# Kernel optimization log

Hardware: AMD Instinct MI355X
Metric: run time of the kernel (lower is better)

The kernel has to match this reference:

```python
import jax, jax.numpy as jnp
import numpy as np

N, E = 50000, 1600000
D_IN, D_HID, D_OUT = 256, 256, 128  # 2*output_dim = 256, output_dim = 128


def glorot(key, shape):
    fan_in, fan_out = shape
    limit = np.sqrt(6.0 / (fan_in + fan_out)).astype(np.float32)
    return jax.random.uniform(key, shape, jnp.float32, -limit, limit)


def setup_inputs() -> dict:
    key = jax.random.key(0)
    k0, k1, k2, k3 = jax.random.split(key, 4)
    x = jax.random.normal(k0, (N, D_IN), jnp.float32)
    edge_index = jax.random.randint(k1, (2, E), 0, N, jnp.int32)
    W1 = glorot(k2, (D_IN, D_HID))
    b1 = jnp.zeros((D_HID,), jnp.float32)
    W2 = glorot(k3, (D_HID, D_OUT))
    b2 = jnp.zeros((D_OUT,), jnp.float32)
    return {"x": x, "edge_index": edge_index, "W1": W1, "b1": b1, "W2": W2, "b2": b2}


def gcn_propagate(x, src, dst, num_nodes):
    """One hop of D^-1/2 (A + I) D^-1/2 @ x (PyG gcn_norm with self-loops)."""
    loops = jnp.arange(num_nodes, dtype=src.dtype)
    src_sl = jnp.concatenate([src, loops])  # [E + N]
    dst_sl = jnp.concatenate([dst, loops])
    ones = jnp.ones(src_sl.shape, x.dtype)
    deg = jax.ops.segment_sum(ones, dst_sl, num_segments=num_nodes)  # >= 1 (self-loop)
    dinv = jax.lax.rsqrt(jnp.maximum(deg, 1e-12))
    norm = dinv[src_sl] * dinv[dst_sl]  # [E + N]
    msgs = x[src_sl] * norm[:, None]    # gather + scale, [E+N, D]
    return jax.ops.segment_sum(msgs, dst_sl, num_segments=num_nodes)


def reference(x, edge_index, W1, b1, W2, b2):
    src, dst = edge_index[0], edge_index[1]
    n = x.shape[0]
    # SGConv(K=1): propagate then linear. conv1 + ReLU
    h = jax.nn.relu(gcn_propagate(x, src, dst, n) @ W1 + b1)
    # conv2 (GAE branch)
    return gcn_propagate(h, src, dst, n) @ W2 + b2
```

## Files before the change

### kernel.cpp

```cpp
#include <hip/hip_runtime.h>

typedef short s16x8 __attribute__((ext_vector_type(8)));
typedef float f32x4 __attribute__((ext_vector_type(4)));
typedef float f32x2 __attribute__((ext_vector_type(2)));

#define TILE 2048

__device__ __forceinline__ unsigned int brne(float f) {
    unsigned int u = __float_as_uint(f);
    return (u + 0x7FFFu + ((u >> 16) & 1u)) >> 16;
}
__device__ __forceinline__ float blo(unsigned int u) { return __uint_as_float(u << 16); }
__device__ __forceinline__ float bhi(unsigned int u) { return __uint_as_float(u & 0xFFFF0000u); }

__device__ __forceinline__ unsigned int pk_bf16(float lo, float hi) {
    unsigned int r;
    asm("v_cvt_pk_bf16_f32 %0, %1, %2" : "=v"(r) : "v"(lo), "v"(hi));
    return r;
}

__device__ __forceinline__ void pkfma(f32x2& a, const f32x2 x, const f32x2 w) {
    asm("v_pk_fma_f32 %0, %1, %2, %0" : "+v"(a) : "v"(x), "v"(w));
}

__device__ __forceinline__ void acc8p(f32x2* a, const uint4 u, const f32x2 w2) {
    pkfma(a[0], (f32x2){blo(u.x), bhi(u.x)}, w2);
    pkfma(a[1], (f32x2){blo(u.y), bhi(u.y)}, w2);
    pkfma(a[2], (f32x2){blo(u.z), bhi(u.z)}, w2);
    pkfma(a[3], (f32x2){blo(u.w), bhi(u.w)}, w2);
}

__device__ __forceinline__ void acc16p(f32x2* a, const uint4 u, const f32x2 w2) {
    pkfma(a[0], __builtin_amdgcn_cvt_pk_f32_fp8((int)u.x, false), w2);
    pkfma(a[1], __builtin_amdgcn_cvt_pk_f32_fp8((int)u.x, true),  w2);
    pkfma(a[2], __builtin_amdgcn_cvt_pk_f32_fp8((int)u.y, false), w2);
    pkfma(a[3], __builtin_amdgcn_cvt_pk_f32_fp8((int)u.y, true),  w2);
    pkfma(a[4], __builtin_amdgcn_cvt_pk_f32_fp8((int)u.z, false), w2);
    pkfma(a[5], __builtin_amdgcn_cvt_pk_f32_fp8((int)u.z, true),  w2);
    pkfma(a[6], __builtin_amdgcn_cvt_pk_f32_fp8((int)u.w, false), w2);
    pkfma(a[7], __builtin_amdgcn_cvt_pk_f32_fp8((int)u.w, true),  w2);
}


__global__ void k_bhist(const int* __restrict__ dst, int* __restrict__ bucket_cnt,
                        int e, int nb) {
    __shared__ int h[256];
    const int tid = threadIdx.x;
    h[tid] = 0;
    __syncthreads();
    const int base = blockIdx.x * TILE + tid;
#pragma unroll
    for (int k = 0; k < 8; k++) {
        const int i = base + k * 256;
        if (i < e) atomicAdd(&h[dst[i] >> 8], 1);
    }
    __syncthreads();
    if (tid < nb && h[tid]) atomicAdd(&bucket_cnt[tid], h[tid]);
}

__global__ void k_bscatter(const int* __restrict__ src, const int* __restrict__ dst,
                           const int* __restrict__ bcnt, int* __restrict__ bbase,
                           int* __restrict__ bcur, uint2* __restrict__ eb, int e, int nb) {
    __shared__ int sh[256], sbase[256], h[256], hbase[256], h2[256];
    const int tid = threadIdx.x;
    const int v = (tid < nb) ? bcnt[tid] : 0;
    int x = v;
    sh[tid] = x;
    __syncthreads();
    for (int off = 1; off < 256; off <<= 1) {
        const int t = (tid >= off) ? sh[tid - off] : 0;
        __syncthreads();
        if (tid >= off) { x += t; sh[tid] = x; }
        __syncthreads();
    }
    sbase[tid] = x - v;
    if (blockIdx.x == 0) {
        if (tid < nb) bbase[tid] = x - v;
        if (tid == 0) bbase[nb] = e;
    }
    h[tid] = 0; h2[tid] = 0;
    __syncthreads();
    const int base = blockIdx.x * TILE + tid;
    int s[8], d[8], b[8];
    bool val[8];
#pragma unroll
    for (int k = 0; k < 8; k++) {
        const int i = base + k * 256;
        val[k] = i < e;
        if (val[k]) {
            s[k] = src[i]; d[k] = dst[i]; b[k] = d[k] >> 8;
            atomicAdd(&h[b[k]], 1);
        }
    }
    __syncthreads();
    if (h[tid]) hbase[tid] = sbase[tid] + atomicAdd(&bcur[tid], h[tid]);
    __syncthreads();
#pragma unroll
    for (int k = 0; k < 8; k++) {
        if (val[k]) {
            const int off = atomicAdd(&h2[b[k]], 1);
            eb[hbase[b[k]] + off] = make_uint2((unsigned)s[k], (unsigned)d[k]);
        }
    }
}

__global__ void k_nhist_scan(const uint2* __restrict__ eb, const int* __restrict__ bucket_base,
                             int* __restrict__ rowptr, int* __restrict__ part,
                             float* __restrict__ dinv, int n) {
    __shared__ int c[256], sh[256];
    const int tid = threadIdx.x, b = blockIdx.x;
    c[tid] = 0;
    __syncthreads();
    const int beg = bucket_base[b], end = bucket_base[b + 1];
    for (int i = beg + tid; i < end; i += 256)
        atomicAdd(&c[eb[i].y & 255], 1);
    __syncthreads();
    const int v = c[tid];
    const int node = b * 256 + tid;
    if (node < n) dinv[node] = rsqrtf((float)(v + 1));
    int x = v;
    sh[tid] = x;
    __syncthreads();
    for (int off = 1; off < 256; off <<= 1) {
        const int t = (tid >= off) ? sh[tid - off] : 0;
        __syncthreads();
        if (tid >= off) { x += t; sh[tid] = x; }
        __syncthreads();
    }
    if (node <= n) rowptr[node] = x - v;
    if (tid == 255) part[b] = x;
}

template <bool PREW>
__global__ void k_place(const uint2* __restrict__ eb, const int* __restrict__ bucket_base,
                        int* __restrict__ rowptr, const int* __restrict__ part,
                        void* __restrict__ esv, const float* __restrict__ dinv,
                        int n, int nb, int e) {
    __shared__ int sh[256], rp[256], offs[256];
    __shared__ float sdv[256];
    const int tid = threadIdx.x, b = blockIdx.x;
    int x = (tid < nb) ? part[tid] : 0;
    sh[tid] = x;
    __syncthreads();
    for (int off = 1; off < 256; off <<= 1) {
        const int t = (tid >= off) ? sh[tid - off] : 0;
        __syncthreads();
        if (tid >= off) { x += t; sh[tid] = x; }
        __syncthreads();
    }
    const int prefix = (b > 0) ? sh[b - 1] : 0;
    const int node = b * 256 + tid;
    int rg = 0;
    if (node <= n) {
        rg = rowptr[node] + prefix;
        rowptr[node] = rg;
    }
    rp[tid] = rg;
    offs[tid] = 0;
    if (PREW) sdv[tid] = (node < n) ? dinv[node] : 0.f;
    __syncthreads();
    const int beg = bucket_base[b], end = bucket_base[b + 1];
    if (PREW) {
        int2* es2 = (int2*)esv;
        if (b == 0 && tid < 64) es2[e + tid] = make_int2(0, 0);
        for (int i = beg + tid; i < end; i += 256) {
            const uint2 ed = eb[i];
            const int sI = (int)ed.x, d = (int)ed.y & 255;
            const float w = dinv[sI] * sdv[d];
            const int local = atomicAdd(&offs[d], 1);
            es2[rp[d] + local] = make_int2(sI, __float_as_int(w));
        }
    } else {
        int* es1 = (int*)esv;
        for (int i = beg + tid; i < end; i += 256) {
            const uint2 ed = eb[i];
            const int d = (int)ed.y & 255;
            const int local = atomicAdd(&offs[d], 1);
            es1[rp[d] + local] = (int)ed.x;
        }
    }
}

__global__ void k_tW2(const float* __restrict__ W1, const float* __restrict__ W2,
                      unsigned short* __restrict__ W1t, unsigned short* __restrict__ W2t) {
    const int t = blockIdx.x * 256 + threadIdx.x;
    if (t < 65536) {
        const int k = t >> 8, nn = t & 255;
        W1t[nn * 256 + k] = (unsigned short)brne(W1[t]);
    } else {
        const int u = t - 65536;
        const int k = u >> 7, nn = u & 127;
        W2t[nn * 256 + k] = (unsigned short)brne(W2[u]);
    }
}

#define LP 40
template <bool AF32, bool FP8OUT>
__global__ __launch_bounds__(256) void k_gemm(const void* __restrict__ Av,
                                              const unsigned short* __restrict__ Bt,
                                              void* __restrict__ Cout,
                                              int M, int Nc) {
    __shared__ unsigned short As[2][128 * LP];
    __shared__ unsigned short Bs[2][128 * LP];

    const int tid = threadIdx.x;
    const int wave = tid >> 6, lane = tid & 63;
    const int wm = (wave >> 1) * 64, wn = (wave & 1) * 64;
    const int l15 = lane & 15, quad = lane >> 4;
    const int mBase = blockIdx.x * 128, nBase = blockIdx.y * 128;

    f32x4 acc[4][4];
#pragma unroll
    for (int i = 0; i < 4; i++)
#pragma unroll
        for (int j = 0; j < 4; j++) acc[i][j] = (f32x4){0.f, 0.f, 0.f, 0.f};

    const int r0 = tid >> 2, kc0 = tid & 3;
    int am0 = mBase + r0;      if (am0 >= M) am0 = M - 1;
    int am1 = mBase + r0 + 64; if (am1 >= M) am1 = M - 1;

    const uint4* Ap0; const uint4* Ap1; const float4* Af0; const float4* Af1;
    if (AF32) {
        Af0 = (const float4*)Av + (size_t)am0 * 64 + kc0 * 2;
        Af1 = (const float4*)Av + (size_t)am1 * 64 + kc0 * 2;
    } else {
        Ap0 = (const uint4*)Av + (size_t)am0 * 32 + kc0;
        Ap1 = (const uint4*)Av + (size_t)am1 * 32 + kc0;
    }
    const uint4* Bp0 = (const uint4*)Bt + (size_t)(nBase + r0) * 32 + kc0;
    const uint4* Bp1 = (const uint4*)Bt + (size_t)(nBase + r0 + 64) * 32 + kc0;

    uint4 a0, a1, b0, b1;
    auto LOAD = [&](int kt) {
        if (AF32) {
            const float4 l0 = Af0[kt * 8], h0 = Af0[kt * 8 + 1];
            const float4 l1 = Af1[kt * 8], h1 = Af1[kt * 8 + 1];
            a0.x = pk_bf16(l0.x, l0.y); a0.y = pk_bf16(l0.z, l0.w);
            a0.z = pk_bf16(h0.x, h0.y); a0.w = pk_bf16(h0.z, h0.w);
            a1.x = pk_bf16(l1.x, l1.y); a1.y = pk_bf16(l1.z, l1.w);
            a1.z = pk_bf16(h1.x, h1.y); a1.w = pk_bf16(h1.z, h1.w);
        } else {
            a0 = Ap0[kt * 4];
            a1 = Ap1[kt * 4];
        }
        b0 = Bp0[kt * 4];
        b1 = Bp1[kt * 4];
    };
    auto STORE = [&](int buf) {
        *(uint4*)&As[buf][r0 * LP + kc0 * 8] = a0;
        *(uint4*)&As[buf][(r0 + 64) * LP + kc0 * 8] = a1;
        *(uint4*)&Bs[buf][r0 * LP + kc0 * 8] = b0;
        *(uint4*)&Bs[buf][(r0 + 64) * LP + kc0 * 8] = b1;
    };

    LOAD(0);
    STORE(0);
    __syncthreads();
    for (int kt = 0; kt < 8; ++kt) {
        const int cur = kt & 1;
        if (kt < 7) LOAD(kt + 1);
        s16x8 af[4], bf[4];
#pragma unroll
        for (int i = 0; i < 4; i++)
            af[i] = *(const s16x8*)&As[cur][(wm + i * 16 + l15) * LP + quad * 8];
#pragma unroll
        for (int j = 0; j < 4; j++)
            bf[j] = *(const s16x8*)&Bs[cur][(wn + j * 16 + l15) * LP + quad * 8];
        if (kt < 7) STORE(cur ^ 1);
#pragma unroll
        for (int i = 0; i < 4; i++)
#pragma unroll
            for (int j = 0; j < 4; j++)
                acc[i][j] = __builtin_amdgcn_mfma_f32_16x16x32_bf16(af[i], bf[j], acc[i][j], 0, 0, 0);
        __syncthreads();
    }

#pragma unroll
    for (int i = 0; i < 4; i++) {
        const int rowb = mBase + wm + i * 16 + quad * 4;
#pragma unroll
        for (int j = 0; j < 4; j++) {
            const int col = nBase + wn + j * 16 + l15;
#pragma unroll
            for (int r = 0; r < 4; r += 2) {
                if (FP8OUT) {
                    const unsigned int pk = __builtin_amdgcn_cvt_pk_fp8_f32(
                        acc[i][j][r], acc[i][j][r + 1], 0, false);
                    if (rowb + r < M)
                        ((unsigned char*)Cout)[(size_t)(rowb + r) * Nc + col] =
                            (unsigned char)pk;
                    if (rowb + r + 1 < M)
                        ((unsigned char*)Cout)[(size_t)(rowb + r + 1) * Nc + col] =
                            (unsigned char)(pk >> 8);
                } else {
                    const unsigned int pk = pk_bf16(acc[i][j][r], acc[i][j][r + 1]);
                    if (rowb + r < M)
                        ((unsigned short*)Cout)[(size_t)(rowb + r) * Nc + col] =
                            (unsigned short)pk;
                    if (rowb + r + 1 < M)
                        ((unsigned short*)Cout)[(size_t)(rowb + r + 1) * Nc + col] =
                            (unsigned short)(pk >> 16);
                }
            }
        }
    }
}


template <bool PREW>
__global__ void k_prop256f8(const uint4* __restrict__ X4,
                            const int* __restrict__ rowptr,
                            const void* __restrict__ esv,
                            const float* __restrict__ dinv,
                            const float* __restrict__ bias,
                            uint4* __restrict__ Y4, int n) {
    const int wid = (int)((blockIdx.x * blockDim.x + threadIdx.x) >> 6);
    const int lane = threadIdx.x & 63;
    const int quad = lane >> 4, l16 = lane & 15;
    if (wid >= n) return;
    const float dd = dinv[wid];
    const int2* es2 = (const int2*)esv;
    const int*  es1 = (const int*)esv;
    f32x2 a[8];
#pragma unroll
    for (int k = 0; k < 8; k++) a[k] = (f32x2){0.f, 0.f};

    const int beg = rowptr[wid], end = rowptr[wid + 1];
    int j = beg + quad;

    auto EDGE = [&](int jj, int& s, float& w) {
        const bool v = jj < end;
        if (PREW) {
            const int2 p = es2[jj];
            s = p.x;
            w = v ? __int_as_float(p.y) : 0.f;
        } else {
            const int idx = v ? jj : 0;
            s = es1[idx];
            w = v ? dinv[s] * dd : 0.f;
        }
    };

    int s0, s1, s2, s3;
    float w0, w1, w2, w3;
    EDGE(j, s0, w0); EDGE(j + 4, s1, w1); EDGE(j + 8, s2, w2); EDGE(j + 12, s3, w3);

    if (quad == 0) {
        const uint4 v = X4[(size_t)wid * 16 + l16];
        acc16p(a, v, (f32x2){dd * dd, dd * dd});
    }

    while (j + 12 < end) {
        const uint4 u0 = X4[(size_t)s0 * 16 + l16];
        const uint4 u1 = X4[(size_t)s1 * 16 + l16];
        const uint4 u2 = X4[(size_t)s2 * 16 + l16];
        const uint4 u3 = X4[(size_t)s3 * 16 + l16];
        j += 16;
        int t0, t1, t2, t3;
        float x0, x1, x2, x3;
        EDGE(j, t0, x0); EDGE(j + 4, t1, x1); EDGE(j + 8, t2, x2); EDGE(j + 12, t3, x3);
        acc16p(a, u0, (f32x2){w0, w0});
        acc16p(a, u1, (f32x2){w1, w1});
        acc16p(a, u2, (f32x2){w2, w2});
        acc16p(a, u3, (f32x2){w3, w3});
        s0 = t0; s1 = t1; s2 = t2; s3 = t3;
        w0 = x0; w1 = x1; w2 = x2; w3 = x3;
    }
    {
        const uint4 u0 = X4[(size_t)s0 * 16 + l16];
        const uint4 u1 = X4[(size_t)s1 * 16 + l16];
        const uint4 u2 = X4[(size_t)s2 * 16 + l16];
        acc16p(a, u0, (f32x2){w0, w0});
        acc16p(a, u1, (f32x2){w1, w1});
        acc16p(a, u2, (f32x2){w2, w2});
    }
#pragma unroll
    for (int k = 0; k < 8; k++) {
        a[k][0] += __shfl_xor(a[k][0], 16);
        a[k][1] += __shfl_xor(a[k][1], 16);
        a[k][0] += __shfl_xor(a[k][0], 32);
        a[k][1] += __shfl_xor(a[k][1], 32);
    }
    if (quad == 0) {
        const float4* bp = (const float4*)bias + l16 * 4;
#pragma unroll
        for (int q = 0; q < 4; q++) {
            const float4 b = bp[q];
            a[2 * q][0]     = fmaxf(a[2 * q][0] + b.x, 0.f);
            a[2 * q][1]     = fmaxf(a[2 * q][1] + b.y, 0.f);
            a[2 * q + 1][0] = fmaxf(a[2 * q + 1][0] + b.z, 0.f);
            a[2 * q + 1][1] = fmaxf(a[2 * q + 1][1] + b.w, 0.f);
        }
        uint4 p0, p1;
        p0.x = pk_bf16(a[0][0], a[0][1]);
        p0.y = pk_bf16(a[1][0], a[1][1]);
        p0.z = pk_bf16(a[2][0], a[2][1]);
        p0.w = pk_bf16(a[3][0], a[3][1]);
        p1.x = pk_bf16(a[4][0], a[4][1]);
        p1.y = pk_bf16(a[5][0], a[5][1]);
        p1.z = pk_bf16(a[6][0], a[6][1]);
        p1.w = pk_bf16(a[7][0], a[7][1]);
        Y4[(size_t)wid * 32 + l16 * 2] = p0;
        Y4[(size_t)wid * 32 + l16 * 2 + 1] = p1;
    }
}

template <bool PREW>
__global__ void k_prop128b(const uint4* __restrict__ X4,
                           const int* __restrict__ rowptr,
                           const void* __restrict__ esv,
                           const float* __restrict__ dinv,
                           const float* __restrict__ bias,
                           float* __restrict__ Yout, int n) {
    const int wid = (int)((blockIdx.x * blockDim.x + threadIdx.x) >> 6);
    const int lane = threadIdx.x & 63;
    const int quad = lane >> 4, l16 = lane & 15;
    if (wid >= n) return;
    const float dd = dinv[wid];
    const int2* es2 = (const int2*)esv;
    const int*  es1 = (const int*)esv;
    f32x2 a[4];
#pragma unroll
    for (int k = 0; k < 4; k++) a[k] = (f32x2){0.f, 0.f};

    const int beg = rowptr[wid], end = rowptr[wid + 1];
    int j = beg + quad;

    auto EDGE = [&](int jj, int& s, float& w) {
        const bool v = jj < end;
        if (PREW) {
            const int2 p = es2[jj];
            s = p.x;
            w = v ? __int_as_float(p.y) : 0.f;
        } else {
            const int idx = v ? jj : 0;
            s = es1[idx];
            w = v ? dinv[s] * dd : 0.f;
        }
    };

    int s0, s1, s2, s3;
    float w0, w1, w2, w3;
    EDGE(j, s0, w0); EDGE(j + 4, s1, w1); EDGE(j + 8, s2, w2); EDGE(j + 12, s3, w3);

    if (quad == 0) {
        const uint4 v = X4[(size_t)wid * 16 + l16];
        acc8p(a, v, (f32x2){dd * dd, dd * dd});
    }

    while (j + 12 < end) {
        const uint4 u0 = X4[(size_t)s0 * 16 + l16];
        const uint4 u1 = X4[(size_t)s1 * 16 + l16];
        const uint4 u2 = X4[(size_t)s2 * 16 + l16];
        const uint4 u3 = X4[(size_t)s3 * 16 + l16];
        j += 16;
        int t0, t1, t2, t3;
        float x0, x1, x2, x3;
        EDGE(j, t0, x0); EDGE(j + 4, t1, x1); EDGE(j + 8, t2, x2); EDGE(j + 12, t3, x3);
        acc8p(a, u0, (f32x2){w0, w0});
        acc8p(a, u1, (f32x2){w1, w1});
        acc8p(a, u2, (f32x2){w2, w2});
        acc8p(a, u3, (f32x2){w3, w3});
        s0 = t0; s1 = t1; s2 = t2; s3 = t3;
        w0 = x0; w1 = x1; w2 = x2; w3 = x3;
    }
    {
        const uint4 u0 = X4[(size_t)s0 * 16 + l16];
        const uint4 u1 = X4[(size_t)s1 * 16 + l16];
        const uint4 u2 = X4[(size_t)s2 * 16 + l16];
        acc8p(a, u0, (f32x2){w0, w0});
        acc8p(a, u1, (f32x2){w1, w1});
        acc8p(a, u2, (f32x2){w2, w2});
    }
#pragma unroll
    for (int k = 0; k < 4; k++) {
        a[k][0] += __shfl_xor(a[k][0], 16);
        a[k][1] += __shfl_xor(a[k][1], 16);
        a[k][0] += __shfl_xor(a[k][0], 32);
        a[k][1] += __shfl_xor(a[k][1], 32);
    }
    if (quad == 0) {
        const float4 b0 = ((const float4*)bias)[l16 * 2];
        const float4 b1 = ((const float4*)bias)[l16 * 2 + 1];
        float4* op = (float4*)Yout + (size_t)wid * 32 + l16 * 2;
        op[0] = make_float4(a[0][0] + b0.x, a[0][1] + b0.y, a[1][0] + b0.z, a[1][1] + b0.w);
        op[1] = make_float4(a[2][0] + b1.x, a[2][1] + b1.y, a[3][0] + b1.z, a[3][1] + b1.w);
    }
}

extern "C" void kernel_launch(void* const* d_in, const int* in_sizes, int n_in,
                              void* d_out, int out_size, void* d_ws, size_t ws_size,
                              hipStream_t stream) {
    const float* x  = (const float*)d_in[0];
    const int*   ei = (const int*)d_in[1];
    const float* W1 = (const float*)d_in[2];
    const float* b1 = (const float*)d_in[3];
    const float* W2 = (const float*)d_in[4];
    const float* b2 = (const float*)d_in[5];
    float* out = (float*)d_out;

    const int n = in_sizes[0] / 256;
    const int e = in_sizes[1] / 2;
    const int* src = ei;
    const int* dst = ei + e;
    const int nb = (n + 255) >> 8;

    auto al = [](size_t v) { return (v + 511) & ~(size_t)511; };
    const size_t fixed = al(sizeof(float) * n) + al(sizeof(int) * (n + 1)) +
                         al(1024) + al(2048) + al(sizeof(int) * 257) +
                         al(2ull * 256 * 256) + al(2ull * 128 * 256) +
                         al((size_t)n * 256) + al(2ull * n * 256) + al(2ull * n * 128);
    const bool prew = (fixed + al(8ull * ((size_t)e + 64))) <= ws_size;

    char* wsp = (char*)d_ws;
    size_t off = 0;
    auto alloc = [&](size_t bytes) -> char* {
        char* p = wsp + off;
        off += (bytes + 511) & ~(size_t)511;
        return p;
    };
    float* dinv    = (float*)alloc(sizeof(float) * n);
    int*   rowptr  = (int*)alloc(sizeof(int) * (n + 1));
    int*   part    = (int*)alloc(1024);
    int*   bcc     = (int*)alloc(2048);
    int*   bcnt    = bcc;
    int*   bcur    = bcc + 256;
    int*   bbase   = (int*)alloc(sizeof(int) * 257);
    void*  es      = (void*)alloc(prew ? 8ull * ((size_t)e + 64) : 4ull * (size_t)e);
    unsigned short* W1t = (unsigned short*)alloc(2ull * 256 * 256);
    unsigned short* W2t = (unsigned short*)alloc(2ull * 128 * 256);
    unsigned char*  T1  = (unsigned char*)alloc((size_t)n * 256);
    unsigned short* H   = (unsigned short*)alloc(2ull * n * 256);
    unsigned short* T2  = (unsigned short*)alloc(2ull * n * 128);
    uint2* eb = (uint2*)H;

    const int nb_t = (e + TILE - 1) / TILE;

    (void)hipMemsetAsync(bcc, 0, 2048, stream);
    k_bhist<<<nb_t, 256, 0, stream>>>(dst, bcnt, e, nb);
    k_bscatter<<<nb_t, 256, 0, stream>>>(src, dst, bcnt, bbase, bcur, eb, e, nb);
    k_nhist_scan<<<nb, 256, 0, stream>>>(eb, bbase, rowptr, part, dinv, n);
    if (prew)
        k_place<true><<<nb, 256, 0, stream>>>(eb, bbase, rowptr, part, es, dinv, n, nb, e);
    else
        k_place<false><<<nb, 256, 0, stream>>>(eb, bbase, rowptr, part, es, dinv, n, nb, e);

    k_tW2<<<(65536 + 32768) / 256, 256, 0, stream>>>(W1, W2, W1t, W2t);

    dim3 g1((n + 127) / 128, 2);
    k_gemm<true, true><<<g1, 256, 0, stream>>>(x, W1t, T1, n, 256);
    if (prew)
        k_prop256f8<true><<<(n + 3) / 4, 256, 0, stream>>>((const uint4*)T1, rowptr, es,
                                                           dinv, b1, (uint4*)H, n);
    else
        k_prop256f8<false><<<(n + 3) / 4, 256, 0, stream>>>((const uint4*)T1, rowptr, es,
                                                            dinv, b1, (uint4*)H, n);

    dim3 g2((n + 127) / 128, 1);
    k_gemm<false, false><<<g2, 256, 0, stream>>>(H, W2t, T2, n, 128);
    if (prew)
        k_prop128b<true><<<(n + 3) / 4, 256, 0, stream>>>((const uint4*)T2, rowptr, es,
                                                          dinv, b2, out, n);
    else
        k_prop128b<false><<<(n + 3) / 4, 256, 0, stream>>>((const uint4*)T2, rowptr, es,
                                                           dinv, b2, out, n);
}
```

Baseline: 318.3 us.

## Replace bucketed two-pass CSR build with global-atomic degree count and direct placement

```diff
diff --git a/kernel.cpp b/kernel.cpp
--- a/kernel.cpp
+++ b/kernel.cpp
@@ -42,81 +42,37 @@
 }
 
 
-__global__ void k_bhist(const int* __restrict__ dst, int* __restrict__ bucket_cnt,
-                        int e, int nb) {
-    __shared__ int h[256];
+__global__ void k_deg_tw(const int* __restrict__ dst, int* __restrict__ deg,
+                         int e, int nbt,
+                         const float* __restrict__ W1, const float* __restrict__ W2,
+                         unsigned short* __restrict__ W1t, unsigned short* __restrict__ W2t) {
     const int tid = threadIdx.x;
-    h[tid] = 0;
-    __syncthreads();
+    if ((int)blockIdx.x >= nbt) {
+        const int t = ((int)blockIdx.x - nbt) * 256 + tid;
+        if (t < 65536) {
+            const int k = t >> 8, nn = t & 255;
+            W1t[nn * 256 + k] = (unsigned short)brne(W1[t]);
+        } else {
+            const int u = t - 65536;
+            const int k = u >> 7, nn = u & 127;
+            W2t[nn * 256 + k] = (unsigned short)brne(W2[u]);
+        }
+        return;
+    }
     const int base = blockIdx.x * TILE + tid;
 #pragma unroll
     for (int k = 0; k < 8; k++) {
         const int i = base + k * 256;
-        if (i < e) atomicAdd(&h[dst[i] >> 8], 1);
-    }
-    __syncthreads();
-    if (tid < nb && h[tid]) atomicAdd(&bucket_cnt[tid], h[tid]);
-}
-
-__global__ void k_bscatter(const int* __restrict__ src, const int* __restrict__ dst,
-                           const int* __restrict__ bcnt, int* __restrict__ bbase,
-                           int* __restrict__ bcur, uint2* __restrict__ eb, int e, int nb) {
-    __shared__ int sh[256], sbase[256], h[256], hbase[256], h2[256];
-    const int tid = threadIdx.x;
-    const int v = (tid < nb) ? bcnt[tid] : 0;
-    int x = v;
-    sh[tid] = x;
-    __syncthreads();
-    for (int off = 1; off < 256; off <<= 1) {
-        const int t = (tid >= off) ? sh[tid - off] : 0;
-        __syncthreads();
-        if (tid >= off) { x += t; sh[tid] = x; }
-        __syncthreads();
-    }
-    sbase[tid] = x - v;
-    if (blockIdx.x == 0) {
-        if (tid < nb) bbase[tid] = x - v;
-        if (tid == 0) bbase[nb] = e;
-    }
-    h[tid] = 0; h2[tid] = 0;
-    __syncthreads();
-    const int base = blockIdx.x * TILE + tid;
-    int s[8], d[8], b[8];
-    bool val[8];
-#pragma unroll
-    for (int k = 0; k < 8; k++) {
-        const int i = base + k * 256;
-        val[k] = i < e;
-        if (val[k]) {
-            s[k] = src[i]; d[k] = dst[i]; b[k] = d[k] >> 8;
-            atomicAdd(&h[b[k]], 1);
-        }
-    }
-    __syncthreads();
-    if (h[tid]) hbase[tid] = sbase[tid] + atomicAdd(&bcur[tid], h[tid]);
-    __syncthreads();
-#pragma unroll
-    for (int k = 0; k < 8; k++) {
-        if (val[k]) {
-            const int off = atomicAdd(&h2[b[k]], 1);
-            eb[hbase[b[k]] + off] = make_uint2((unsigned)s[k], (unsigned)d[k]);
-        }
-    }
-}
-
-__global__ void k_nhist_scan(const uint2* __restrict__ eb, const int* __restrict__ bucket_base,
-                             int* __restrict__ rowptr, int* __restrict__ part,
-                             float* __restrict__ dinv, int n) {
-    __shared__ int c[256], sh[256];
+        if (i < e) atomicAdd(&deg[dst[i]], 1);
+    }
+}
+
+__global__ void k_scan1(const int* __restrict__ deg, int* __restrict__ rowptr,
+                        int* __restrict__ part, float* __restrict__ dinv, int n) {
+    __shared__ int sh[256];
     const int tid = threadIdx.x, b = blockIdx.x;
-    c[tid] = 0;
-    __syncthreads();
-    const int beg = bucket_base[b], end = bucket_base[b + 1];
-    for (int i = beg + tid; i < end; i += 256)
-        atomicAdd(&c[eb[i].y & 255], 1);
-    __syncthreads();
-    const int v = c[tid];
     const int node = b * 256 + tid;
+    const int v = (node < n) ? deg[node] : 0;
     if (node < n) dinv[node] = rsqrtf((float)(v + 1));
     int x = v;
     sh[tid] = x;
@@ -132,12 +88,9 @@
 }
 
 template <bool PREW>
-__global__ void k_place(const uint2* __restrict__ eb, const int* __restrict__ bucket_base,
-                        int* __restrict__ rowptr, const int* __restrict__ part,
-                        void* __restrict__ esv, const float* __restrict__ dinv,
-                        int n, int nb, int e) {
-    __shared__ int sh[256], rp[256], offs[256];
-    __shared__ float sdv[256];
+__global__ void k_scan2(int* __restrict__ rowptr, const int* __restrict__ part,
+                        void* __restrict__ esv, int n, int nb, int e) {
+    __shared__ int sh[256];
     const int tid = threadIdx.x, b = blockIdx.x;
     int x = (tid < nb) ? part[tid] : 0;
     sh[tid] = x;
@@ -150,47 +103,28 @@
     }
     const int prefix = (b > 0) ? sh[b - 1] : 0;
     const int node = b * 256 + tid;
-    int rg = 0;
-    if (node <= n) {
-        rg = rowptr[node] + prefix;
-        rowptr[node] = rg;
-    }
-    rp[tid] = rg;
-    offs[tid] = 0;
-    if (PREW) sdv[tid] = (node < n) ? dinv[node] : 0.f;
-    __syncthreads();
-    const int beg = bucket_base[b], end = bucket_base[b + 1];
-    if (PREW) {
-        int2* es2 = (int2*)esv;
-        if (b == 0 && tid < 64) es2[e + tid] = make_int2(0, 0);
-        for (int i = beg + tid; i < end; i += 256) {
-            const uint2 ed = eb[i];
-            const int sI = (int)ed.x, d = (int)ed.y & 255;
-            const float w = dinv[sI] * sdv[d];
-            const int local = atomicAdd(&offs[d], 1);
-            es2[rp[d] + local] = make_int2(sI, __float_as_int(w));
-        }
-    } else {
-        int* es1 = (int*)esv;
-        for (int i = beg + tid; i < end; i += 256) {
-            const uint2 ed = eb[i];
-            const int d = (int)ed.y & 255;
-            const int local = atomicAdd(&offs[d], 1);
-            es1[rp[d] + local] = (int)ed.x;
-        }
-    }
-}
-
-__global__ void k_tW2(const float* __restrict__ W1, const float* __restrict__ W2,
-                      unsigned short* __restrict__ W1t, unsigned short* __restrict__ W2t) {
-    const int t = blockIdx.x * 256 + threadIdx.x;
-    if (t < 65536) {
-        const int k = t >> 8, nn = t & 255;
-        W1t[nn * 256 + k] = (unsigned short)brne(W1[t]);
-    } else {
-        const int u = t - 65536;
-        const int k = u >> 7, nn = u & 127;
-        W2t[nn * 256 + k] = (unsigned short)brne(W2[u]);
+    if (node <= n && prefix) rowptr[node] += prefix;
+    if (PREW && b == 0 && tid < 64) ((int2*)esv)[e + tid] = make_int2(0, 0);
+}
+
+template <bool PREW>
+__global__ void k_place2(const int* __restrict__ src, const int* __restrict__ dst,
+                         const int* __restrict__ rowptr, int* __restrict__ cur,
+                         const float* __restrict__ dinv, void* __restrict__ esv, int e) {
+    const int base = blockIdx.x * TILE + threadIdx.x;
+#pragma unroll
+    for (int k = 0; k < 8; k++) {
+        const int i = base + k * 256;
+        if (i < e) {
+            const int s = src[i], d = dst[i];
+            const int slot = rowptr[d] + atomicAdd(&cur[d], 1);
+            if (PREW) {
+                const float w = dinv[s] * dinv[d];
+                ((int2*)esv)[slot] = make_int2(s, __float_as_int(w));
+            } else {
+                ((int*)esv)[slot] = s;
+            }
+        }
     }
 }
 
@@ -330,13 +264,13 @@
 
     auto EDGE = [&](int jj, int& s, float& w) {
         const bool v = jj < end;
+        const int idx = v ? jj : beg;
         if (PREW) {
-            const int2 p = es2[jj];
+            const int2 p = es2[idx];
             s = p.x;
             w = v ? __int_as_float(p.y) : 0.f;
         } else {
-            const int idx = v ? jj : 0;
-            s = es1[idx];
+            s = es1[v ? jj : 0];
             w = v ? dinv[s] * dd : 0.f;
         }
     };
@@ -428,13 +362,13 @@
 
     auto EDGE = [&](int jj, int& s, float& w) {
         const bool v = jj < end;
+        const int idx = v ? jj : beg;
         if (PREW) {
-            const int2 p = es2[jj];
+            const int2 p = es2[idx];
             s = p.x;
             w = v ? __int_as_float(p.y) : 0.f;
         } else {
-            const int idx = v ? jj : 0;
-            s = es1[idx];
+            s = es1[v ? jj : 0];
             w = v ? dinv[s] * dd : 0.f;
         }
     };
@@ -507,7 +441,7 @@
 
     auto al = [](size_t v) { return (v + 511) & ~(size_t)511; };
     const size_t fixed = al(sizeof(float) * n) + al(sizeof(int) * (n + 1)) +
-                         al(1024) + al(2048) + al(sizeof(int) * 257) +
+                         al(1024) + al(8ull * n) +
                          al(2ull * 256 * 256) + al(2ull * 128 * 256) +
                          al((size_t)n * 256) + al(2ull * n * 256) + al(2ull * n * 128);
     const bool prew = (fixed + al(8ull * ((size_t)e + 64))) <= ws_size;
@@ -522,30 +456,29 @@
     float* dinv    = (float*)alloc(sizeof(float) * n);
     int*   rowptr  = (int*)alloc(sizeof(int) * (n + 1));
     int*   part    = (int*)alloc(1024);
-    int*   bcc     = (int*)alloc(2048);
-    int*   bcnt    = bcc;
-    int*   bcur    = bcc + 256;
-    int*   bbase   = (int*)alloc(sizeof(int) * 257);
+    int*   degcur  = (int*)alloc(8ull * n);
+    int*   deg     = degcur;
+    int*   cur     = degcur + n;
     void*  es      = (void*)alloc(prew ? 8ull * ((size_t)e + 64) : 4ull * (size_t)e);
     unsigned short* W1t = (unsigned short*)alloc(2ull * 256 * 256);
     unsigned short* W2t = (unsigned short*)alloc(2ull * 128 * 256);
     unsigned char*  T1  = (unsigned char*)alloc((size_t)n * 256);
     unsigned short* H   = (unsigned short*)alloc(2ull * n * 256);
     unsigned short* T2  = (unsigned short*)alloc(2ull * n * 128);
-    uint2* eb = (uint2*)H;
 
     const int nb_t = (e + TILE - 1) / TILE;
-
-    (void)hipMemsetAsync(bcc, 0, 2048, stream);
-    k_bhist<<<nb_t, 256, 0, stream>>>(dst, bcnt, e, nb);
-    k_bscatter<<<nb_t, 256, 0, stream>>>(src, dst, bcnt, bbase, bcur, eb, e, nb);
-    k_nhist_scan<<<nb, 256, 0, stream>>>(eb, bbase, rowptr, part, dinv, n);
-    if (prew)
-        k_place<true><<<nb, 256, 0, stream>>>(eb, bbase, rowptr, part, es, dinv, n, nb, e);
-    else
-        k_place<false><<<nb, 256, 0, stream>>>(eb, bbase, rowptr, part, es, dinv, n, nb, e);
-
-    k_tW2<<<(65536 + 32768) / 256, 256, 0, stream>>>(W1, W2, W1t, W2t);
+    const int tw_b = (65536 + 32768) / 256;
+
+    (void)hipMemsetAsync(degcur, 0, 8ull * n, stream);
+    k_deg_tw<<<nb_t + tw_b, 256, 0, stream>>>(dst, deg, e, nb_t, W1, W2, W1t, W2t);
+    k_scan1<<<nb, 256, 0, stream>>>(deg, rowptr, part, dinv, n);
+    if (prew) {
+        k_scan2<true><<<nb, 256, 0, stream>>>(rowptr, part, es, n, nb, e);
+        k_place2<true><<<nb_t, 256, 0, stream>>>(src, dst, rowptr, cur, dinv, es, e);
+    } else {
+        k_scan2<false><<<nb, 256, 0, stream>>>(rowptr, part, es, n, nb, e);
+        k_place2<false><<<nb_t, 256, 0, stream>>>(src, dst, rowptr, cur, dinv, es, e);
+    }
 
     dim3 g1((n + 127) / 128, 2);
     k_gemm<true, true><<<g1, 256, 0, stream>>>(x, W1t, T1, n, 256);
```

After: 407.9 us. 28.1% more time.
